# Optimization experiments

Hardware: AMD Instinct MI355X
Metric: run time of the kernel (lower is better)

The kernel has to match this reference:

```python
import jax, jax.numpy as jnp
import numpy as np

NN = 262144        # total nodes = 4096 graphs * 64 nodes
EN = 524288        # directed edges
IN_DIM = 32
H = 128
PROP_STEPS = 3


def setup_inputs() -> dict:
    key = jax.random.key(0)
    ks = jax.random.split(key, 16)
    s = lambda d: 1.0 / np.sqrt(d)
    x = jax.random.normal(ks[0], (NN, IN_DIM), dtype=jnp.float32)
    # edges: random within each 64-node graph block would be most faithful; random
    # over NN is the same access pattern workload-wise. Use per-graph-local edges.
    src = jax.random.randint(ks[1], (EN,), 0, NN, dtype=jnp.int64)
    dst = jax.random.randint(ks[2], (EN,), 0, NN, dtype=jnp.int64)
    edge_index = jnp.stack([src, dst], axis=0)
    return {
        "x": x,
        "edge_index": edge_index,
        "W_in": jax.random.normal(ks[3], (IN_DIM, H), jnp.float32) * s(IN_DIM),
        "b_in": jnp.zeros((H,), jnp.float32),
        "W_e1": jax.random.normal(ks[4], (H, H), jnp.float32) * s(H),
        "b_e1": jnp.zeros((H,), jnp.float32),
        "W_e2": jax.random.normal(ks[5], (H, H), jnp.float32) * s(H),
        "b_e2": jnp.zeros((H,), jnp.float32),
        "W_ih": jax.random.normal(ks[6], (H, 3 * H), jnp.float32) * s(H),
        "b_ih": jnp.zeros((3 * H,), jnp.float32),
        "W_hh": jax.random.normal(ks[7], (H, 3 * H), jnp.float32) * s(H),
        "b_hh": jnp.zeros((3 * H,), jnp.float32),
        "W_out": jax.random.normal(ks[8], (H, 1), jnp.float32) * s(H),
        "b_out": jnp.zeros((1,), jnp.float32),
    }


def reference(x, edge_index, W_in, b_in, W_e1, b_e1, W_e2, b_e2,
              W_ih, b_ih, W_hh, b_hh, W_out, b_out):
    in_node, out_node = edge_index[0], edge_index[1]
    nn = x.shape[0]
    # input MLP: Linear + tanh
    h = jnp.tanh(x @ W_in + b_in)                         # [NN, H]
    for _ in range(PROP_STEPS):
        # unified edge MLP (hidden tanh + linear out), applied per node then gathered
        m = jnp.tanh(h @ W_e1 + b_e1) @ W_e2 + b_e2       # [NN, H]
        msg = m[in_node]                                  # [EN, H] gather
        ssum = jax.ops.segment_sum(msg, out_node, num_segments=nn)
        cnt = jax.ops.segment_sum(jnp.ones((msg.shape[0],), msg.dtype),
                                  out_node, num_segments=nn)
        m_agg = ssum / jnp.maximum(cnt, 1.0)[:, None]     # scatter_mean, [NN, H]
        # GRU cell update: input = m_agg, hidden = h (torch GRUCell math)
        gi = m_agg @ W_ih + b_ih                          # [NN, 3H]
        gh = h @ W_hh + b_hh                              # [NN, 3H]
        i_r, i_z, i_n = jnp.split(gi, 3, axis=-1)
        h_r, h_z, h_n = jnp.split(gh, 3, axis=-1)
        r = jax.nn.sigmoid(i_r + h_r)
        z = jax.nn.sigmoid(i_z + h_z)
        n = jnp.tanh(i_n + r * h_n)
        h = (1.0 - z) * n + z * h
    # unified output head: single Linear
    return h @ W_out + b_out                              # [NN, 1]
```

## Files before the change

### kernel.cpp

```cpp
#include <hip/hip_runtime.h>

#define NN 262144
#define EN 524288
#define HD 128
#define IND 32

#define NT    (NN/64)
#define GRID_G 512
#define GRID_E 768

typedef __attribute__((ext_vector_type(8))) short s16x8;
typedef __attribute__((ext_vector_type(4))) float f32x4;
typedef unsigned short u16;
typedef unsigned int u32;

#define MFMA(a,b,c) __builtin_amdgcn_mfma_f32_16x16x32_bf16(a,b,c,0,0,0)
#define SWZ(p) ((p) ^ ((((p)>>8)&7)<<4))

typedef __attribute__((address_space(1))) void gas_void;
typedef __attribute__((address_space(3))) void las_void;
__device__ __forceinline__ void gload16(const void* g, void* l){
  __builtin_amdgcn_global_load_lds((gas_void*)g, (las_void*)l, 16, 0, 0);
}

__device__ __forceinline__ u16 f2b(float f){
  u32 u = __builtin_bit_cast(u32, f);
  u = (u + 0x7fffu + ((u >> 16) & 1u)) >> 16;
  return (u16)u;
}
__device__ __forceinline__ float b2f(u32 lo16){ return __builtin_bit_cast(float, lo16 << 16); }
__device__ __forceinline__ float rcpf_(float x){ return __builtin_amdgcn_rcpf(x); }
__device__ __forceinline__ float fsig(float x){ return rcpf_(1.f + __expf(-x)); }
__device__ __forceinline__ float ftanh(float x){ return 1.f - 2.f*rcpf_(1.f + __expf(2.f*x)); }

__global__ __launch_bounds__(256) void k_w2bt(const float* __restrict__ W, u16* __restrict__ Wt, int K, int N){
  int idx = blockIdx.x*256 + threadIdx.x;
  if (idx >= K*N) return;
  int n = idx / K, k = idx - n*K;
  Wt[idx] = f2b(W[k*N + n]);
}

__global__ void k_eflag(const int* __restrict__ ei, int* __restrict__ flag){
  int v = ei[threadIdx.x*2 + 1];
  unsigned long long b = __ballot(v != 0);
  if (threadIdx.x == 0) flag[0] = (b == 0ULL) ? 1 : 0;
}
__device__ __forceinline__ int eget(const int* ei, int f, int which, int e){
  return f ? ei[(which*EN + e)*2] : ei[which*EN + e];
}

__global__ __launch_bounds__(256) void k_count(const int* __restrict__ ei, const int* __restrict__ flag, int* __restrict__ cnt){
  int e = blockIdx.x*256 + threadIdx.x;
  if (e < EN) atomicAdd(&cnt[eget(ei, flag[0], 1, e)], 1);
}
__global__ __launch_bounds__(256) void k_scan1(const int* __restrict__ cnt, int* __restrict__ excl, int* __restrict__ bsum){
  __shared__ int ws[4];
  int i = blockIdx.x*256 + threadIdx.x;
  int v = cnt[i];
  int ln = threadIdx.x & 63;
  int x = v;
  #pragma unroll
  for (int d=1; d<64; d<<=1){ int y = __shfl_up(x, d); if (ln >= d) x += y; }
  if (ln == 63) ws[threadIdx.x>>6] = x;
  __syncthreads();
  int wpre = 0;
  for (int j=0; j<(threadIdx.x>>6); ++j) wpre += ws[j];
  excl[i] = wpre + x - v;
  if (threadIdx.x == 255) bsum[blockIdx.x] = wpre + x;
}
__global__ __launch_bounds__(1024) void k_scan2(int* __restrict__ bsum){
  __shared__ int ws[16];
  int i = threadIdx.x;
  int v = bsum[i];
  int ln = i & 63;
  int x = v;
  #pragma unroll
  for (int d=1; d<64; d<<=1){ int y = __shfl_up(x, d); if (ln >= d) x += y; }
  if (ln == 63) ws[i>>6] = x;
  __syncthreads();
  int wpre = 0;
  for (int j=0; j<(i>>6); ++j) wpre += ws[j];
  bsum[i] = wpre + x - v;
}
__global__ __launch_bounds__(256) void k_scan3(const int* __restrict__ excl, const int* __restrict__ bsum, int* __restrict__ rp, int* __restrict__ cur){
  int i = blockIdx.x*256 + threadIdx.x;
  int v = excl[i] + bsum[blockIdx.x];
  rp[i] = v; cur[i] = v;
  if (i == 0) rp[NN] = EN;
}
__global__ __launch_bounds__(256) void k_fill(const int* __restrict__ ei, const int* __restrict__ flag, int* __restrict__ cur, int* __restrict__ cx){
  int e = blockIdx.x*256 + threadIdx.x;
  if (e >= EN) return;
  int f = flag[0];
  int p = atomicAdd(&cur[eget(ei, f, 1, e)], 1);
  cx[p] = eget(ei, f, 0, e);
}

__global__ __launch_bounds__(256) void k_input(const float* __restrict__ x, const u16* __restrict__ wt, const float* __restrict__ bias, u16* __restrict__ h){
  const int wv = threadIdx.x >> 6, ln = threadIdx.x & 63;
  const int l15 = ln & 15, lg = ln >> 4;
  const int base = blockIdx.x*128 + wv*32;
  s16x8 a[2];
  #pragma unroll
  for (int rt=0; rt<2; ++rt){
    const float* xp = x + (base + rt*16 + l15)*IND + lg*8;
    float4 v0 = *reinterpret_cast<const float4*>(xp);
    float4 v1 = *reinterpret_cast<const float4*>(xp + 4);
    s16x8 t;
    t[0]=(short)f2b(v0.x); t[1]=(short)f2b(v0.y); t[2]=(short)f2b(v0.z); t[3]=(short)f2b(v0.w);
    t[4]=(short)f2b(v1.x); t[5]=(short)f2b(v1.y); t[6]=(short)f2b(v1.z); t[7]=(short)f2b(v1.w);
    a[rt] = t;
  }
  #pragma unroll
  for (int cg=0; cg<8; ++cg){
    const int col = cg*16 + l15;
    s16x8 bf = *reinterpret_cast<const s16x8*>(wt + col*IND + lg*8);
    float bb = bias[col];
    f32x4 acc0 = {bb,bb,bb,bb}, acc1 = {bb,bb,bb,bb};
    acc0 = MFMA(a[0], bf, acc0);
    acc1 = MFMA(a[1], bf, acc1);
    #pragma unroll
    for (int r=0; r<4; ++r){
      h[(base + lg*4 + r)*HD + col]      = f2b(ftanh(acc0[r]));
      h[(base + 16 + lg*4 + r)*HD + col] = f2b(ftanh(acc1[r]));
    }
  }
}

__global__ __launch_bounds__(512) void k_edge(const u16* __restrict__ h, const u16* __restrict__ wt1, const float* __restrict__ b1,
                                              const u16* __restrict__ wt2, const float* __restrict__ b2, u16* __restrict__ m){
  extern __shared__ __align__(1024) unsigned char lds[];
  const int tid = threadIdx.x, wv = tid >> 6, ln = tid & 63;
  const int l15 = ln & 15, lg = ln >> 4;
  const int col = wv*16 + l15;

  s16x8 B1[4], B2[4];
  #pragma unroll
  for (int kk=0; kk<4; ++kk){
    const int ko = kk*32 + lg*8;
    B1[kk] = *reinterpret_cast<const s16x8*>(wt1 + (size_t)col*HD + ko);
    B2[kk] = *reinterpret_cast<const s16x8*>(wt2 + (size_t)col*HD + ko);
  }
  const float b1s = b1[col], b2s = b2[col];

  {
    const unsigned char* hg = (const unsigned char*)h + (size_t)blockIdx.x*64*256;
    #pragma unroll
    for (int i=0; i<2; ++i){
      int c = wv*2 + i;
      int p = c*1024 + ln*16;
      gload16(hg + SWZ(p), lds + c*1024);
    }
  }
  __syncthreads();

  unsigned char* tl = lds + 32768;
  int t = 0;
  #pragma unroll 1
  for (int tt = blockIdx.x; tt < NT; tt += GRID_E, ++t){
    if (tt + GRID_E < NT){
      const unsigned char* hg = (const unsigned char*)h + (size_t)(tt+GRID_E)*64*256;
      unsigned char* dst = lds + ((t+1)&1)*16384;
      #pragma unroll
      for (int i=0; i<2; ++i){
        int c = wv*2 + i;
        int p = c*1024 + ln*16;
        gload16(hg + SWZ(p), dst + c*1024);
      }
    }
    const unsigned char* hl = lds + (t&1)*16384;
    for (int rt=0; rt<4; ++rt){
      s16x8 a[4];
      #pragma unroll
      for (int kk=0; kk<4; ++kk){
        int row = rt*16 + l15;
        int p = row*256 + (((kk*4+lg) ^ (row&7))<<4);
        a[kk] = *reinterpret_cast<const s16x8*>(hl + p);
      }
      f32x4 acc = {b1s,b1s,b1s,b1s};
      __builtin_amdgcn_s_setprio(1);
      #pragma unroll
      for (int kk=0; kk<4; ++kk) acc = MFMA(a[kk], B1[kk], acc);
      __builtin_amdgcn_s_setprio(0);
      #pragma unroll
      for (int r=0; r<4; ++r){
        int row = rt*16 + lg*4 + r;
        int tb = row*256 + ((((col*2)>>4) ^ (row&7))<<4) + ((col&7)*2);
        *reinterpret_cast<u16*>(tl + tb) = f2b(ftanh(acc[r]));
      }
    }
    __syncthreads();
    for (int rt=0; rt<4; ++rt){
      s16x8 a[4];
      #pragma unroll
      for (int kk=0; kk<4; ++kk){
        int row = rt*16 + l15;
        int p = row*256 + (((kk*4+lg) ^ (row&7))<<4);
        a[kk] = *reinterpret_cast<const s16x8*>(tl + p);
      }
      f32x4 acc = {b2s,b2s,b2s,b2s};
      __builtin_amdgcn_s_setprio(1);
      #pragma unroll
      for (int kk=0; kk<4; ++kk) acc = MFMA(a[kk], B2[kk], acc);
      __builtin_amdgcn_s_setprio(0);
      #pragma unroll
      for (int r=0; r<4; ++r){
        int row = rt*16 + lg*4 + r;
        m[(size_t)(tt*64+row)*HD + col] = f2b(acc[r]);
      }
    }
    __syncthreads();
  }
}

__global__ __launch_bounds__(256) void k_agg(const u16* __restrict__ m, const int* __restrict__ rp, const int* __restrict__ cx, u16* __restrict__ magg){
  const int wv = threadIdx.x >> 6, ln = threadIdx.x & 63;
  const int n = blockIdx.x*4 + wv;
  int s0 = rp[n], s1 = rp[n+1];
  float a0 = 0.f, a1 = 0.f;
  int p = s0;
  for (; p + 2 <= s1; p += 2){
    int na = cx[p], nb = cx[p+1];
    u32 va = *reinterpret_cast<const u32*>(m + (size_t)na*HD + ln*2);
    u32 vb = *reinterpret_cast<const u32*>(m + (size_t)nb*HD + ln*2);
    a0 += b2f(va & 0xffffu) + b2f(vb & 0xffffu);
    a1 += b2f(va >> 16)     + b2f(vb >> 16);
  }
  if (p < s1){
    int na = cx[p];
    u32 va = *reinterpret_cast<const u32*>(m + (size_t)na*HD + ln*2);
    a0 += b2f(va & 0xffffu);
    a1 += b2f(va >> 16);
  }
  int deg = s1 - s0;
  float inv = rcpf_((float)(deg > 0 ? deg : 1));
  u32 o = (u32)f2b(a0*inv) | ((u32)f2b(a1*inv) << 16);
  *reinterpret_cast<u32*>(magg + n*HD + ln*2) = o;
}

__global__ __launch_bounds__(512) void k_gru(const u16* __restrict__ magg, u16* __restrict__ h,
    const u16* __restrict__ wtih, const float* __restrict__ bih,
    const u16* __restrict__ wthh, const float* __restrict__ bhh){
  extern __shared__ __align__(1024) unsigned char lds[];
  const int tid = threadIdx.x, wv = tid >> 6, ln = tid & 63;
  const int l15 = ln & 15, lg = ln >> 4;
  const int col = wv*16 + l15;

  s16x8 B[6][4];
  #pragma unroll
  for (int kk=0; kk<4; ++kk){
    const int ko = kk*32 + lg*8;
    B[0][kk] = *reinterpret_cast<const s16x8*>(wtih + (size_t)(col       )*HD + ko);
    B[1][kk] = *reinterpret_cast<const s16x8*>(wtih + (size_t)(col +   HD)*HD + ko);
    B[2][kk] = *reinterpret_cast<const s16x8*>(wtih + (size_t)(col + 2*HD)*HD + ko);
    B[3][kk] = *reinterpret_cast<const s16x8*>(wthh + (size_t)(col       )*HD + ko);
    B[4][kk] = *reinterpret_cast<const s16x8*>(wthh + (size_t)(col +   HD)*HD + ko);
    B[5][kk] = *reinterpret_cast<const s16x8*>(wthh + (size_t)(col + 2*HD)*HD + ko);
  }
  const float brz = bih[col] + bhh[col];
  const float bzz = bih[col+HD] + bhh[col+HD];
  const float bin_ = bih[col+2*HD], bhn_ = bhh[col+2*HD];

  {
    const unsigned char* mg = (const unsigned char*)magg + (size_t)blockIdx.x*64*256;
    const unsigned char* hg = (const unsigned char*)h    + (size_t)blockIdx.x*64*256;
    #pragma unroll
    for (int i=0; i<4; ++i){
      int c = wv*4 + i;
      int p = (c & 15)*1024 + ln*16;
      gload16((c < 16 ? mg : hg) + SWZ(p), lds + c*1024);
    }
  }
  __syncthreads();

  int t = 0;
  #pragma unroll 1
  for (int tt = blockIdx.x; tt < NT; tt += GRID_G, ++t){
    if (tt + GRID_G < NT){
      const unsigned char* mg = (const unsigned char*)magg + (size_t)(tt+GRID_G)*64*256;
      const unsigned char* hg = (const unsigned char*)h    + (size_t)(tt+GRID_G)*64*256;
      unsigned char* dst = lds + ((t+1)&1)*32768;
      #pragma unroll
      for (int i=0; i<4; ++i){
        int c = wv*4 + i;
        int p = (c & 15)*1024 + ln*16;
        gload16((c < 16 ? mg : hg) + SWZ(p), dst + c*1024);
      }
    }
    const unsigned char* mgl = lds + (t&1)*32768;
    const unsigned char* hl  = mgl + 16384;

    for (int rt=0; rt<4; ++rt){
      s16x8 amg[4], ahh[4];
      #pragma unroll
      for (int kk=0; kk<4; ++kk){
        int row = rt*16 + l15;
        int p = row*256 + (((kk*4+lg) ^ (row&7))<<4);
        amg[kk] = *reinterpret_cast<const s16x8*>(mgl + p);
        ahh[kk] = *reinterpret_cast<const s16x8*>(hl + p);
      }
      f32x4 ir = {brz,brz,brz,brz}, iz = {bzz,bzz,bzz,bzz}, inn = {bin_,bin_,bin_,bin_};
      f32x4 hr = {0.f,0.f,0.f,0.f}, hz = {0.f,0.f,0.f,0.f}, hn  = {bhn_,bhn_,bhn_,bhn_};
      __builtin_amdgcn_s_setprio(1);
      #pragma unroll
      for (int kk=0; kk<4; ++kk){
        ir  = MFMA(amg[kk], B[0][kk], ir);
        iz  = MFMA(amg[kk], B[1][kk], iz);
        inn = MFMA(amg[kk], B[2][kk], inn);
        hr  = MFMA(ahh[kk], B[3][kk], hr);
        hz  = MFMA(ahh[kk], B[4][kk], hz);
        hn  = MFMA(ahh[kk], B[5][kk], hn);
      }
      __builtin_amdgcn_s_setprio(0);
      #pragma unroll
      for (int r=0; r<4; ++r){
        int row = rt*16 + lg*4 + r;
        int ce = col & ~1;
        int hb = row*256 + ((((ce*2)>>4) ^ (row&7))<<4) + ((ce&7)*2);
        u32 pair = *reinterpret_cast<const u32*>(hl + hb);
        float hold = __builtin_bit_cast(float, (col&1) ? (pair & 0xffff0000u) : (pair << 16));
        float rg = fsig(ir[r] + hr[r]);
        float zg = fsig(iz[r] + hz[r]);
        float ng = ftanh(inn[r] + rg*hn[r]);
        h[(size_t)(tt*64+row)*HD + col] = f2b(ng + zg*(hold - ng));
      }
    }
    __syncthreads();
  }
}

__global__ __launch_bounds__(256) void k_out(const u16* __restrict__ h, const float* __restrict__ wo, const float* __restrict__ bo, float* __restrict__ out){
  const int wv = threadIdx.x >> 6, ln = threadIdx.x & 63;
  const int n = (blockIdx.x*4 + wv)*4 + (ln >> 4);
  const int kc = (ln & 15)*8;
  uint4 v = *reinterpret_cast<const uint4*>(h + n*HD + kc);
  float4 w0 = *reinterpret_cast<const float4*>(wo + kc);
  float4 w1 = *reinterpret_cast<const float4*>(wo + kc + 4);
  float s = b2f(v.x & 0xffffu)*w0.x + b2f(v.x >> 16)*w0.y + b2f(v.y & 0xffffu)*w0.z + b2f(v.y >> 16)*w0.w
          + b2f(v.z & 0xffffu)*w1.x + b2f(v.z >> 16)*w1.y + b2f(v.w & 0xffffu)*w1.z + b2f(v.w >> 16)*w1.w;
  #pragma unroll
  for (int d=1; d<16; d<<=1) s += __shfl_xor(s, d, 16);
  if ((ln & 15) == 0) out[n] = s + bo[0];
}

#define AL256(x) ((((size_t)(x)) + 255) & ~(size_t)255)
static const size_t SZ_STATE = (size_t)NN*HD*2;
static const size_t OFF_H    = 0;
static const size_t OFF_M    = OFF_H + SZ_STATE;
static const size_t OFF_MAGG = OFF_M + SZ_STATE;
static const size_t OFF_RP   = OFF_MAGG + SZ_STATE;
static const size_t OFF_CUR  = OFF_RP + AL256((size_t)(NN+1)*4);
static const size_t OFF_CNT  = OFF_CUR + (size_t)NN*4;
static const size_t OFF_EXCL = OFF_CNT + (size_t)NN*4;
static const size_t OFF_BSUM = OFF_EXCL + (size_t)NN*4;
static const size_t OFF_CX   = OFF_BSUM + AL256(1024*4);
static const size_t OFF_FLAG = OFF_CX + (size_t)EN*4;
static const size_t OFF_WTIN = OFF_FLAG + 256;
static const size_t OFF_WTE1 = OFF_WTIN + AL256((size_t)IND*HD*2);
static const size_t OFF_WTE2 = OFF_WTE1 + AL256((size_t)HD*HD*2);
static const size_t OFF_WTIH = OFF_WTE2 + AL256((size_t)HD*HD*2);
static const size_t OFF_WTHH = OFF_WTIH + AL256((size_t)HD*3*HD*2);

extern "C" void kernel_launch(void* const* d_in, const int* in_sizes, int n_in,
                              void* d_out, int out_size, void* d_ws, size_t ws_size,
                              hipStream_t stream){
  const float* x    = (const float*)d_in[0];
  const int*   ei   = (const int*)d_in[1];
  const float* W_in = (const float*)d_in[2];  const float* b_in = (const float*)d_in[3];
  const float* W_e1 = (const float*)d_in[4];  const float* b_e1 = (const float*)d_in[5];
  const float* W_e2 = (const float*)d_in[6];  const float* b_e2 = (const float*)d_in[7];
  const float* W_ih = (const float*)d_in[8];  const float* b_ih = (const float*)d_in[9];
  const float* W_hh = (const float*)d_in[10]; const float* b_hh = (const float*)d_in[11];
  const float* W_out= (const float*)d_in[12]; const float* b_out= (const float*)d_in[13];
  float* out = (float*)d_out;

  char* ws = (char*)d_ws;
  u16* h    = (u16*)(ws + OFF_H);
  u16* m    = (u16*)(ws + OFF_M);
  u16* magg = (u16*)(ws + OFF_MAGG);
  int* rp   = (int*)(ws + OFF_RP);
  int* cur  = (int*)(ws + OFF_CUR);
  int* cnt  = (int*)(ws + OFF_CNT);
  int* excl = (int*)(ws + OFF_EXCL);
  int* bsum = (int*)(ws + OFF_BSUM);
  int* cx   = (int*)(ws + OFF_CX);
  int* flag = (int*)(ws + OFF_FLAG);
  u16* wtin = (u16*)(ws + OFF_WTIN);
  u16* wte1 = (u16*)(ws + OFF_WTE1);
  u16* wte2 = (u16*)(ws + OFF_WTE2);
  u16* wtih = (u16*)(ws + OFF_WTIH);
  u16* wthh = (u16*)(ws + OFF_WTHH);

  hipFuncSetAttribute((const void*)k_edge, hipFuncAttributeMaxDynamicSharedMemorySize, 49152);
  hipFuncSetAttribute((const void*)k_gru,  hipFuncAttributeMaxDynamicSharedMemorySize, 65536);

  hipMemsetAsync(cnt, 0, (size_t)NN*4, stream);

  k_w2bt<<<(IND*HD + 255)/256, 256, 0, stream>>>(W_in, wtin, IND, HD);
  k_w2bt<<<(HD*HD + 255)/256, 256, 0, stream>>>(W_e1, wte1, HD, HD);
  k_w2bt<<<(HD*HD + 255)/256, 256, 0, stream>>>(W_e2, wte2, HD, HD);
  k_w2bt<<<(HD*3*HD + 255)/256, 256, 0, stream>>>(W_ih, wtih, HD, 3*HD);
  k_w2bt<<<(HD*3*HD + 255)/256, 256, 0, stream>>>(W_hh, wthh, HD, 3*HD);

  k_eflag<<<1, 64, 0, stream>>>(ei, flag);
  k_count<<<EN/256, 256, 0, stream>>>(ei, flag, cnt);
  k_scan1<<<NN/256, 256, 0, stream>>>(cnt, excl, bsum);
  k_scan2<<<1, 1024, 0, stream>>>(bsum);
  k_scan3<<<NN/256, 256, 0, stream>>>(excl, bsum, rp, cur);
  k_fill<<<EN/256, 256, 0, stream>>>(ei, flag, cur, cx);

  k_input<<<NN/128, 256, 0, stream>>>(x, wtin, b_in, h);

  for (int it=0; it<3; ++it){
    k_edge<<<GRID_E, 512, 49152, stream>>>(h, wte1, b_e1, wte2, b_e2, m);
    k_agg<<<NN/4, 256, 0, stream>>>(m, rp, cx, magg);
    k_gru<<<GRID_G, 512, 65536, stream>>>(magg, h, wtih, b_ih, wthh, b_hh);
  }
  k_out<<<NN/16, 256, 0, stream>>>(h, W_out, b_out, out);
}
```

Before: 614.8 us.

## Widen GRU tiles to 128 rows with software-pipelined MFMA/epilogue and half-wave aggregation

The GRU kernel now processes 128-row tiles with 128 KB double-buffered LDS, and software-pipelines the row sub-tiles so each sub-tile's loads and MFMAs overlap the previous one's gate epilogue. The r/z input and hidden contributions are accumulated into shared accumulators, which drops two accumulator sets. The aggregation kernel gives each node 32 lanes loading 8 bytes instead of 64 lanes loading 4 bytes, halving the wave count. The larger LDS footprint lowers occupancy to one block per CU, and the extra live registers from the pipelined sub-tiles may cause register pressure.

```diff
diff --git a/kernel.cpp b/kernel.cpp
--- a/kernel.cpp
+++ b/kernel.cpp
@@ -5,9 +5,10 @@
 #define HD 128
 #define IND 32
 
-#define NT    (NN/64)
-#define GRID_G 512
+#define NT64  (NN/64)
 #define GRID_E 768
+#define NT128 (NN/128)
+#define GRID_G 256
 
 typedef __attribute__((ext_vector_type(8))) short s16x8;
 typedef __attribute__((ext_vector_type(4))) float f32x4;
@@ -157,8 +158,8 @@
   unsigned char* tl = lds + 32768;
   int t = 0;
   #pragma unroll 1
-  for (int tt = blockIdx.x; tt < NT; tt += GRID_E, ++t){
-    if (tt + GRID_E < NT){
+  for (int tt = blockIdx.x; tt < NT64; tt += GRID_E, ++t){
+    if (tt + GRID_E < NT64){
       const unsigned char* hg = (const unsigned char*)h + (size_t)(tt+GRID_E)*64*256;
       unsigned char* dst = lds + ((t+1)&1)*16384;
       #pragma unroll
@@ -214,28 +215,32 @@
 }
 
 __global__ __launch_bounds__(256) void k_agg(const u16* __restrict__ m, const int* __restrict__ rp, const int* __restrict__ cx, u16* __restrict__ magg){
-  const int wv = threadIdx.x >> 6, ln = threadIdx.x & 63;
-  const int n = blockIdx.x*4 + wv;
+  const int sub = threadIdx.x >> 5, l32 = threadIdx.x & 31;
+  const int n = blockIdx.x*8 + sub;
   int s0 = rp[n], s1 = rp[n+1];
-  float a0 = 0.f, a1 = 0.f;
+  float a0=0.f, a1=0.f, a2=0.f, a3=0.f;
   int p = s0;
   for (; p + 2 <= s1; p += 2){
     int na = cx[p], nb = cx[p+1];
-    u32 va = *reinterpret_cast<const u32*>(m + (size_t)na*HD + ln*2);
-    u32 vb = *reinterpret_cast<const u32*>(m + (size_t)nb*HD + ln*2);
-    a0 += b2f(va & 0xffffu) + b2f(vb & 0xffffu);
-    a1 += b2f(va >> 16)     + b2f(vb >> 16);
+    uint2 va = *reinterpret_cast<const uint2*>(m + (size_t)na*HD + l32*4);
+    uint2 vb = *reinterpret_cast<const uint2*>(m + (size_t)nb*HD + l32*4);
+    a0 += b2f(va.x & 0xffffu) + b2f(vb.x & 0xffffu);
+    a1 += b2f(va.x >> 16)     + b2f(vb.x >> 16);
+    a2 += b2f(va.y & 0xffffu) + b2f(vb.y & 0xffffu);
+    a3 += b2f(va.y >> 16)     + b2f(vb.y >> 16);
   }
   if (p < s1){
     int na = cx[p];
-    u32 va = *reinterpret_cast<const u32*>(m + (size_t)na*HD + ln*2);
-    a0 += b2f(va & 0xffffu);
-    a1 += b2f(va >> 16);
+    uint2 va = *reinterpret_cast<const uint2*>(m + (size_t)na*HD + l32*4);
+    a0 += b2f(va.x & 0xffffu); a1 += b2f(va.x >> 16);
+    a2 += b2f(va.y & 0xffffu); a3 += b2f(va.y >> 16);
   }
   int deg = s1 - s0;
   float inv = rcpf_((float)(deg > 0 ? deg : 1));
-  u32 o = (u32)f2b(a0*inv) | ((u32)f2b(a1*inv) << 16);
-  *reinterpret_cast<u32*>(magg + n*HD + ln*2) = o;
+  uint2 o;
+  o.x = (u32)f2b(a0*inv) | ((u32)f2b(a1*inv) << 16);
+  o.y = (u32)f2b(a2*inv) | ((u32)f2b(a3*inv) << 16);
+  *reinterpret_cast<uint2*>(magg + (size_t)n*HD + l32*4) = o;
 }
 
 __global__ __launch_bounds__(512) void k_gru(const u16* __restrict__ magg, u16* __restrict__ h,
@@ -245,6 +250,7 @@
   const int tid = threadIdx.x, wv = tid >> 6, ln = tid & 63;
   const int l15 = ln & 15, lg = ln >> 4;
   const int col = wv*16 + l15;
+  const int ce = col & ~1;
 
   s16x8 B[6][4];
   #pragma unroll
@@ -262,71 +268,90 @@
   const float bin_ = bih[col+2*HD], bhn_ = bhh[col+2*HD];
 
   {
-    const unsigned char* mg = (const unsigned char*)magg + (size_t)blockIdx.x*64*256;
-    const unsigned char* hg = (const unsigned char*)h    + (size_t)blockIdx.x*64*256;
+    const unsigned char* mg = (const unsigned char*)magg + (size_t)blockIdx.x*128*256;
+    const unsigned char* hg = (const unsigned char*)h    + (size_t)blockIdx.x*128*256;
     #pragma unroll
-    for (int i=0; i<4; ++i){
-      int c = wv*4 + i;
-      int p = (c & 15)*1024 + ln*16;
-      gload16((c < 16 ? mg : hg) + SWZ(p), lds + c*1024);
+    for (int i=0; i<8; ++i){
+      int c = wv*8 + i;
+      int p = (c & 31)*1024 + ln*16;
+      gload16((c < 32 ? mg : hg) + SWZ(p), lds + c*1024);
     }
   }
   __syncthreads();
+
+#define LOADA(rt, amg, ahh, hld) { \
+    const int row_ = (rt)*16 + l15; \
+    _Pragma("unroll") \
+    for (int kk=0; kk<4; ++kk){ \
+      int p_ = row_*256 + (((kk*4+lg) ^ (row_&7))<<4); \
+      amg[kk] = *reinterpret_cast<const s16x8*>(mgl + p_); \
+      ahh[kk] = *reinterpret_cast<const s16x8*>(hl + p_); } \
+    _Pragma("unroll") \
+    for (int r_=0; r_<4; ++r_){ \
+      int hrow_ = (rt)*16 + lg*4 + r_; \
+      int hb_ = hrow_*256 + ((((ce*2)>>4) ^ (hrow_&7))<<4) + ((ce&7)*2); \
+      hld[r_] = *reinterpret_cast<const u32*>(hl + hb_); } }
+
+#define MFMAS(amg, ahh, aR, aZ, aN, aH) { \
+    aR = (f32x4){brz,brz,brz,brz}; aZ = (f32x4){bzz,bzz,bzz,bzz}; \
+    aN = (f32x4){bin_,bin_,bin_,bin_}; aH = (f32x4){bhn_,bhn_,bhn_,bhn_}; \
+    __builtin_amdgcn_s_setprio(1); \
+    _Pragma("unroll") \
+    for (int kk=0; kk<4; ++kk){ \
+      aR = MFMA(amg[kk], B[0][kk], aR); \
+      aZ = MFMA(amg[kk], B[1][kk], aZ); \
+      aN = MFMA(amg[kk], B[2][kk], aN); \
+      aH = MFMA(ahh[kk], B[5][kk], aH); \
+      aR = MFMA(ahh[kk], B[3][kk], aR); \
+      aZ = MFMA(ahh[kk], B[4][kk], aZ); } \
+    __builtin_amdgcn_s_setprio(0); }
+
+#define EPI(rt, aR, aZ, aN, aH, hld) { \
+    _Pragma("unroll") \
+    for (int r_=0; r_<4; ++r_){ \
+      int row_ = (rt)*16 + lg*4 + r_; \
+      float hold_ = __builtin_bit_cast(float, (col&1) ? (hld[r_] & 0xffff0000u) : (hld[r_] << 16)); \
+      float rg_ = fsig(aR[r_]); \
+      float zg_ = fsig(aZ[r_]); \
+      float ng_ = ftanh(aN[r_] + rg_*aH[r_]); \
+      h[(size_t)(tt*128+row_)*HD + col] = f2b(ng_ + zg_*(hold_ - ng_)); } }
 
   int t = 0;
   #pragma unroll 1
-  for (int tt = blockIdx.x; tt < NT; tt += GRID_G, ++t){
-    if (tt + GRID_G < NT){
-      const unsigned char* mg = (const unsigned char*)magg + (size_t)(tt+GRID_G)*64*256;
-      const unsigned char* hg = (const unsigned char*)h    + (size_t)(tt+GRID_G)*64*256;
-      unsigned char* dst = lds + ((t+1)&1)*32768;
-      #pragma unroll
-      for (int i=0; i<4; ++i){
-        int c = wv*4 + i;
-        int p = (c & 15)*1024 + ln*16;
-        gload16((c < 16 ? mg : hg) + SWZ(p), dst + c*1024);
-      }
-    }
-    const unsigned char* mgl = lds + (t&1)*32768;
-    const unsigned char* hl  = mgl + 16384;
-
-    for (int rt=0; rt<4; ++rt){
-      s16x8 amg[4], ahh[4];
-      #pragma unroll
-      for (int kk=0; kk<4; ++kk){
-        int row = rt*16 + l15;
-        int p = row*256 + (((kk*4+lg) ^ (row&7))<<4);
-        amg[kk] = *reinterpret_cast<const s16x8*>(mgl + p);
-        ahh[kk] = *reinterpret_cast<const s16x8*>(hl + p);
-      }
-      f32x4 ir = {brz,brz,brz,brz}, iz = {bzz,bzz,bzz,bzz}, inn = {bin_,bin_,bin_,bin_};
-      f32x4 hr = {0.f,0.f,0.f,0.f}, hz = {0.f,0.f,0.f,0.f}, hn  = {bhn_,bhn_,bhn_,bhn_};
-      __builtin_amdgcn_s_setprio(1);
-      #pragma unroll
-      for (int kk=0; kk<4; ++kk){
-        ir  = MFMA(amg[kk], B[0][kk], ir);
-        iz  = MFMA(amg[kk], B[1][kk], iz);
-        inn = MFMA(amg[kk], B[2][kk], inn);
-        hr  = MFMA(ahh[kk], B[3][kk], hr);
-        hz  = MFMA(ahh[kk], B[4][kk], hz);
-        hn  = MFMA(ahh[kk], B[5][kk], hn);
-      }
-      __builtin_amdgcn_s_setprio(0);
-      #pragma unroll
-      for (int r=0; r<4; ++r){
-        int row = rt*16 + lg*4 + r;
-        int ce = col & ~1;
-        int hb = row*256 + ((((ce*2)>>4) ^ (row&7))<<4) + ((ce&7)*2);
-        u32 pair = *reinterpret_cast<const u32*>(hl + hb);
-        float hold = __builtin_bit_cast(float, (col&1) ? (pair & 0xffff0000u) : (pair << 16));
-        float rg = fsig(ir[r] + hr[r]);
-        float zg = fsig(iz[r] + hz[r]);
-        float ng = ftanh(inn[r] + rg*hn[r]);
-        h[(size_t)(tt*64+row)*HD + col] = f2b(ng + zg*(hold - ng));
-      }
-    }
+  for (int tt = blockIdx.x; tt < NT128; tt += GRID_G, ++t){
+    if (tt + GRID_G < NT128){
+      const unsigned char* mg = (const unsigned char*)magg + (size_t)(tt+GRID_G)*128*256;
+      const unsigned char* hg = (const unsigned char*)h    + (size_t)(tt+GRID_G)*128*256;
+      unsigned char* dst = lds + ((t+1)&1)*65536;
+      #pragma unroll
+      for (int i=0; i<8; ++i){
+        int c = wv*8 + i;
+        int p = (c & 31)*1024 + ln*16;
+        gload16((c < 32 ? mg : hg) + SWZ(p), dst + c*1024);
+      }
+    }
+    const unsigned char* mgl = lds + (t&1)*65536;
+    const unsigned char* hl  = mgl + 32768;
+
+    s16x8 amgA[4], ahhA[4], amgB[4], ahhB[4];
+    u32 hldA[4], hldB[4];
+    f32x4 rA, zA, nA, hA, rB, zB, nB, hB;
+
+    LOADA(0, amgA, ahhA, hldA); MFMAS(amgA, ahhA, rA, zA, nA, hA);
+    LOADA(1, amgB, ahhB, hldB); MFMAS(amgB, ahhB, rB, zB, nB, hB); EPI(0, rA, zA, nA, hA, hldA);
+    LOADA(2, amgA, ahhA, hldA); MFMAS(amgA, ahhA, rA, zA, nA, hA); EPI(1, rB, zB, nB, hB, hldB);
+    LOADA(3, amgB, ahhB, hldB); MFMAS(amgB, ahhB, rB, zB, nB, hB); EPI(2, rA, zA, nA, hA, hldA);
+    LOADA(4, amgA, ahhA, hldA); MFMAS(amgA, ahhA, rA, zA, nA, hA); EPI(3, rB, zB, nB, hB, hldB);
+    LOADA(5, amgB, ahhB, hldB); MFMAS(amgB, ahhB, rB, zB, nB, hB); EPI(4, rA, zA, nA, hA, hldA);
+    LOADA(6, amgA, ahhA, hldA); MFMAS(amgA, ahhA, rA, zA, nA, hA); EPI(5, rB, zB, nB, hB, hldB);
+    LOADA(7, amgB, ahhB, hldB); MFMAS(amgB, ahhB, rB, zB, nB, hB); EPI(6, rA, zA, nA, hA, hldA);
+    EPI(7, rB, zB, nB, hB, hldB);
+
     __syncthreads();
   }
+#undef LOADA
+#undef MFMAS
+#undef EPI
 }
 
 __global__ __launch_bounds__(256) void k_out(const u16* __restrict__ h, const float* __restrict__ wo, const float* __restrict__ bo, float* __restrict__ out){
@@ -392,7 +417,7 @@
   u16* wthh = (u16*)(ws + OFF_WTHH);
 
   hipFuncSetAttribute((const void*)k_edge, hipFuncAttributeMaxDynamicSharedMemorySize, 49152);
-  hipFuncSetAttribute((const void*)k_gru,  hipFuncAttributeMaxDynamicSharedMemorySize, 65536);
+  hipFuncSetAttribute((const void*)k_gru,  hipFuncAttributeMaxDynamicSharedMemorySize, 131072);
 
   hipMemsetAsync(cnt, 0, (size_t)NN*4, stream);
 
@@ -413,8 +438,8 @@
 
   for (int it=0; it<3; ++it){
     k_edge<<<GRID_E, 512, 49152, stream>>>(h, wte1, b_e1, wte2, b_e2, m);
-    k_agg<<<NN/4, 256, 0, stream>>>(m, rp, cx, magg);
-    k_gru<<<GRID_G, 512, 65536, stream>>>(magg, h, wtih, b_ih, wthh, b_hh);
+    k_agg<<<NN/8, 256, 0, stream>>>(m, rp, cx, magg);
+    k_gru<<<GRID_G, 512, 131072, stream>>>(magg, h, wtih, b_ih, wthh, b_hh);
   }
   k_out<<<NN/16, 256, 0, stream>>>(h, W_out, b_out, out);
 }
```

New measurement: 534.4 us. 13.1% less time.
